# Optimization experiments

Hardware: AMD Instinct MI355X
Metric: run time of the kernel (lower is better)

## Reference

```python
import jax, jax.numpy as jnp
import numpy as np
from jax import lax

L, B, S, D, H = 2, 8, 2048, 1024, 1024
LOG_H0 = float(np.log(0.5))  # h0 = g(0) = 0.5


def _log_g(x):
    # log of g(x) = x + 0.5 if x >= 0 else sigmoid(x)
    return jnp.where(x >= 0, jnp.log(jnp.where(x >= 0, x + 0.5, 1.0)), -jax.nn.softplus(-x))


def _mingru_layer(x, Wz, bz, Wh, bh):
    # x: (B,S,D) -> (B,S,H) via log-space heinsen associative scan
    k = jnp.einsum('bsd,hd->bsh', x, Wz) + bz          # gate pre-activation
    log_z = -jax.nn.softplus(-k)                        # log sigmoid(k)
    log_coeffs = -jax.nn.softplus(k)                    # log (1 - sigmoid(k))
    pre_h = jnp.einsum('bsd,hd->bsh', x, Wh) + bh
    log_values = log_z + _log_g(pre_h)                  # log(z * h_tilde)
    Bq = x.shape[0]
    # prepend initial state: coeff 0 (log 1), value log(h0)
    log_coeffs = jnp.pad(log_coeffs, ((0, 0), (1, 0), (0, 0)))
    log_values = jnp.concatenate(
        [jnp.full((Bq, 1, log_values.shape[-1]), LOG_H0, dtype=log_values.dtype), log_values], axis=1)
    a_star = jnp.cumsum(log_coeffs, axis=1)
    log_h = a_star + lax.cumlogsumexp(log_values - a_star, axis=1)
    return jnp.exp(log_h)[:, 1:]


def setup_inputs() -> dict:
    key = jax.random.key(0)
    ks = jax.random.split(key, 5)
    stdv = 1.0 / np.sqrt(D)
    u = lambda k, shp: jax.random.uniform(k, shp, jnp.float32, -stdv, stdv)
    return {
        'x': jax.random.normal(ks[0], (B, S, D), jnp.float32),
        'Wz': u(ks[1], (L, H, D)),
        'bz': u(ks[2], (L, H)),
        'Wh': u(ks[3], (L, H, D)),
        'bh': u(ks[4], (L, H)),
    }


def reference(x, Wz, bz, Wh, bh):
    h = x
    for l in range(Wz.shape[0]):
        h = _mingru_layer(h, Wz[l], bz[l], Wh[l], bh[l])
    return h  # (B,S,H), last layer outputs
```

## Files before the change

kernel.cpp:

```cpp
#include <hip/hip_runtime.h>
#include <hip/hip_bf16.h>


#define L_ 2
#define B_ 8
#define S_ 2048
#define D_ 1024
#define H_ 1024
#define M_ (B_*S_)
#define NC 32
#define CL (S_/NC)

typedef __bf16    bf16x8 __attribute__((ext_vector_type(8)));
typedef float     f32x4  __attribute__((ext_vector_type(4)));
typedef _Float16  h2     __attribute__((ext_vector_type(2)));
typedef _Float16  h4     __attribute__((ext_vector_type(4)));

__device__ __forceinline__ ushort f2bf(float f) {
    union { __hip_bfloat16 h; ushort u; } c;
    c.h = __float2bfloat16(f);
    return c.u;
}

__device__ __forceinline__ void async16(const void* g, void* l) {
    __builtin_amdgcn_global_load_lds(
        (const __attribute__((address_space(1))) unsigned int*)g,
        (__attribute__((address_space(3))) unsigned int*)l, 16, 0, 0);
}

__global__ __launch_bounds__(256) void cast_f32_bf16(const float* __restrict__ in,
                                                     ushort* __restrict__ out, int n4) {
    int i = blockIdx.x * 256 + threadIdx.x;
    if (i >= n4) return;
    float4 v = ((const float4*)in)[i];
    ushort4 o;
    o.x = f2bf(v.x); o.y = f2bf(v.y); o.z = f2bf(v.z); o.w = f2bf(v.w);
    ((ushort4*)out)[i] = o;
}

#define SWZ(R, c) (((R) << 6) + ((((c) ^ ((R) & 7))) << 3))

__global__ __launch_bounds__(256) void gemm_fused(const ushort* __restrict__ A,
                                                  const ushort* __restrict__ Wz,
                                                  const ushort* __restrict__ Wh,
                                                  const float* __restrict__ bz,
                                                  const float* __restrict__ bh,
                                                  h2* __restrict__ cv,
                                                  float* __restrict__ Ac,
                                                  float* __restrict__ Bc)
{
    __shared__ __align__(16) ushort sm[16384];
    ushort* As = sm;
    ushort* Zs = sm + 8192;
    ushort* Hs = sm + 12288;

    const int t    = threadIdx.x;
    const int lane = t & 63;
    const int wave = t >> 6;
    const int xcd = (int)blockIdx.x & 7;
    const int k8  = (int)blockIdx.x >> 3;
    const int nblk = k8 & 15;
    const int mblk = ((k8 >> 4) << 3) + xcd;
    const int m0 = mblk * 128;
    const int n0 = nblk * 64;
    const int wm = (wave >> 1) * 64;
    const int wn = (wave & 1) * 32;

    const int srow   = lane >> 3;
    const int scol_g = (((lane & 7) ^ srow) << 3);

    f32x4 accz[4][2] = {};
    f32x4 acch[4][2] = {};
    const int lrow = lane & 15;
    const int lcq  = lane >> 4;

    for (int kb = 0; kb < D_; kb += 64) {
        __syncthreads();
        #pragma unroll
        for (int i = 0; i < 4; ++i) {
            int r = i*32 + wave*8;
            async16(&A[(size_t)(m0 + r + srow)*D_ + kb + scol_g], &As[r*64]);
        }
        #pragma unroll
        for (int i = 0; i < 2; ++i) {
            int r = i*32 + wave*8;
            async16(&Wz[(size_t)(n0 + r + srow)*D_ + kb + scol_g], &Zs[r*64]);
            async16(&Wh[(size_t)(n0 + r + srow)*D_ + kb + scol_g], &Hs[r*64]);
        }
        __syncthreads();
        #pragma unroll
        for (int kk = 0; kk < 64; kk += 32) {
            const int cq = (kk >> 3) + lcq;
            bf16x8 af[4];
            #pragma unroll
            for (int mt = 0; mt < 4; ++mt) {
                int R = wm + mt*16 + lrow;
                uint4 u = *(const uint4*)&As[SWZ(R, cq)];
                af[mt] = __builtin_bit_cast(bf16x8, u);
            }
            #pragma unroll
            for (int nt = 0; nt < 2; ++nt) {
                int R = wn + nt*16 + lrow;
                uint4 uz = *(const uint4*)&Zs[SWZ(R, cq)];
                uint4 uh = *(const uint4*)&Hs[SWZ(R, cq)];
                bf16x8 zb = __builtin_bit_cast(bf16x8, uz);
                bf16x8 hb = __builtin_bit_cast(bf16x8, uh);
                #pragma unroll
                for (int mt = 0; mt < 4; ++mt) {
                    accz[mt][nt] = __builtin_amdgcn_mfma_f32_16x16x32_bf16(af[mt], zb, accz[mt][nt], 0, 0, 0);
                    acch[mt][nt] = __builtin_amdgcn_mfma_f32_16x16x32_bf16(af[mt], hb, acch[mt][nt], 0, 0, 0);
                }
            }
        }
    }

    __syncthreads();
    float2* seg = (float2*)sm;

    const int colq = lane & 15;
    const int rowq = (lane >> 4) * 4;
    #pragma unroll
    for (int nt = 0; nt < 2; ++nt) {
        const int n = n0 + wn + nt*16 + colq;
        const float bzv = bz[n];
        const float bhv = bh[n];
        #pragma unroll
        for (int mt = 0; mt < 4; ++mt) {
            float a = 1.f, bb = 0.f;
            #pragma unroll
            for (int r = 0; r < 4; ++r) {
                const int m = m0 + wm + mt*16 + rowq + r;
                float k = accz[mt][nt][r] + bzv;
                float p = acch[mt][nt][r] + bhv;
                float e   = __expf(-fabsf(k));
                float inv = 1.0f / (1.0f + e);
                float z   = (k >= 0.f) ? inv     : e * inv;
                float c   = (k >= 0.f) ? e * inv : inv;
                float g;
                if (p >= 0.f) g = p + 0.5f;
                else { float eg = __expf(p); g = eg / (1.0f + eg); }
                float v = z * g;
                h2 hv; hv[0] = (_Float16)c; hv[1] = (_Float16)v;
                cv[(size_t)m * H_ + n] = hv;
                bb = fmaf(c, bb, v);
                a *= c;
            }
            const int sidx = (wm >> 2) + mt*4 + (rowq >> 2);
            seg[sidx*65 + wn + nt*16 + colq] = make_float2(a, bb);
        }
    }
    __syncthreads();
    if (t < 128) {
        const int col  = t & 63;
        const int half = t >> 6;
        float a = 1.f, bb = 0.f;
        #pragma unroll
        for (int s = 0; s < 16; ++s) {
            float2 e = seg[(half*16 + s)*65 + col];
            bb = fmaf(e.x, bb, e.y);
            a *= e.x;
        }
        const int b     = m0 >> 11;
        const int chunk = ((m0 >> 6) & (NC - 1)) + half;
        const int q = (b*NC + chunk)*H_ + n0 + col;
        Ac[q] = a; Bc[q] = bb;
    }
}

__global__ __launch_bounds__(256) void scan_chunk_combine(const float* __restrict__ Ac,
                                                          const float* __restrict__ Bc,
                                                          float* __restrict__ hin)
{
    int q = blockIdx.x * 256 + threadIdx.x;
    int h = q & (H_-1);
    int b = q >> 10;
    float hcur = 0.5f;
    #pragma unroll
    for (int c = 0; c < NC; ++c) {
        int idx = (b*NC + c)*H_ + h;
        hin[idx] = hcur;
        hcur = fmaf(Ac[idx], hcur, Bc[idx]);
    }
}

__global__ __launch_bounds__(256) void scan_emit(const h2* __restrict__ cv,
                                                 const float* __restrict__ hin,
                                                 float* __restrict__ outf,
                                                 ushort* __restrict__ outb,
                                                 const int write_bf16)
{
    int q = blockIdx.x * 256 + threadIdx.x;
    int hp = (q & 511) * 2;
    int c = (q >> 9) & (NC-1);
    int b = q >> 14;
    size_t base = (size_t)(b*S_ + c*CL) * H_ + hp;
    int qh = (b*NC + c)*H_ + hp;
    float h0 = hin[qh], h1 = hin[qh + 1];
    if (write_bf16) {
        #pragma unroll 4
        for (int tt = 0; tt < CL; ++tt) {
            h4 e = *(const h4*)&cv[base + (size_t)tt * H_];
            h0 = fmaf((float)e[0], h0, (float)e[1]);
            h1 = fmaf((float)e[2], h1, (float)e[3]);
            ushort2 o; o.x = f2bf(h0); o.y = f2bf(h1);
            *(ushort2*)&outb[base + (size_t)tt * H_] = o;
        }
    } else {
        #pragma unroll 4
        for (int tt = 0; tt < CL; ++tt) {
            h4 e = *(const h4*)&cv[base + (size_t)tt * H_];
            h0 = fmaf((float)e[0], h0, (float)e[1]);
            h1 = fmaf((float)e[2], h1, (float)e[3]);
            *(float2*)&outf[base + (size_t)tt * H_] = make_float2(h0, h1);
        }
    }
}

extern "C" void kernel_launch(void* const* d_in, const int* in_sizes, int n_in,
                              void* d_out, int out_size, void* d_ws, size_t ws_size,
                              hipStream_t stream)
{
    const float* x  = (const float*)d_in[0];
    const float* Wz = (const float*)d_in[1];
    const float* bz = (const float*)d_in[2];
    const float* Wh = (const float*)d_in[3];
    const float* bh = (const float*)d_in[4];
    float* out = (float*)d_out;

    ushort* xb  = (ushort*)d_ws;
    ushort* wzb = xb  + (size_t)M_*D_;
    ushort* whb = wzb + (size_t)L_*H_*D_;
    h2*     cv  = (h2*)(whb + (size_t)L_*H_*D_);
    float*  Ac  = (float*)(cv + (size_t)M_*H_);
    float*  Bc  = Ac + B_*NC*H_;
    float*  hin = Bc + B_*NC*H_;

    cast_f32_bf16<<<(M_*D_/4)/256, 256, 0, stream>>>(x, xb, M_*D_/4);
    cast_f32_bf16<<<(L_*H_*D_/4)/256, 256, 0, stream>>>(Wz, wzb, L_*H_*D_/4);
    cast_f32_bf16<<<(L_*H_*D_/4)/256, 256, 0, stream>>>(Wh, whb, L_*H_*D_/4);

    const int gemm_grid = (M_/128) * (H_/64);
    for (int l = 0; l < L_; ++l) {
        gemm_fused<<<gemm_grid, 256, 0, stream>>>(xb,
                                                  wzb + (size_t)l*H_*D_,
                                                  whb + (size_t)l*H_*D_,
                                                  bz + l*H_, bh + l*H_,
                                                  cv, Ac, Bc);
        scan_chunk_combine<<<(B_*H_)/256, 256, 0, stream>>>(Ac, Bc, hin);
        scan_emit<<<(B_*NC*H_/2)/256, 256, 0, stream>>>(cv, hin, out, xb, (l == 0) ? 1 : 0);
    }
}
```

Baseline: 340.8 us.

## Store gate coefficient/value pairs time-major per channel for vectorized writes and scan reads

The intermediate (coefficient, value) fp16 pairs move from a [b,t,h] layout to a [b,h,t] layout. The GEMM epilogue can then pack four consecutive timesteps into one 16-byte store instead of four scattered 4-byte stores. The scan kernel reads 16-byte runs along time for each channel. The catch is that adjacent threads in the scan now read addresses S apart, so each thread's loads are wide but not coalesced across the warp.

Measured after the change: 353.2 us. 3.7% more time.

```diff
diff --git a/kernel.cpp b/kernel.cpp
--- a/kernel.cpp
+++ b/kernel.cpp
@@ -14,7 +14,6 @@
 typedef __bf16    bf16x8 __attribute__((ext_vector_type(8)));
 typedef float     f32x4  __attribute__((ext_vector_type(4)));
 typedef _Float16  h2     __attribute__((ext_vector_type(2)));
-typedef _Float16  h4     __attribute__((ext_vector_type(4)));
 
 __device__ __forceinline__ ushort f2bf(float f) {
     union { __hip_bfloat16 h; ushort u; } c;
@@ -119,6 +118,8 @@
 
     const int colq = lane & 15;
     const int rowq = (lane >> 4) * 4;
+    const int bq   = m0 >> 11;
+    const int tb   = m0 & (S_-1);
     #pragma unroll
     for (int nt = 0; nt < 2; ++nt) {
         const int n = n0 + wn + nt*16 + colq;
@@ -127,9 +128,9 @@
         #pragma unroll
         for (int mt = 0; mt < 4; ++mt) {
             float a = 1.f, bb = 0.f;
+            union { h2 h[4]; uint4 u; } pk;
             #pragma unroll
             for (int r = 0; r < 4; ++r) {
-                const int m = m0 + wm + mt*16 + rowq + r;
                 float k = accz[mt][nt][r] + bzv;
                 float p = acch[mt][nt][r] + bhv;
                 float e   = __expf(-fabsf(k));
@@ -140,11 +141,12 @@
                 if (p >= 0.f) g = p + 0.5f;
                 else { float eg = __expf(p); g = eg / (1.0f + eg); }
                 float v = z * g;
-                h2 hv; hv[0] = (_Float16)c; hv[1] = (_Float16)v;
-                cv[(size_t)m * H_ + n] = hv;
+                pk.h[r][0] = (_Float16)c; pk.h[r][1] = (_Float16)v;
                 bb = fmaf(c, bb, v);
                 a *= c;
             }
+            const int tt = tb + wm + mt*16 + rowq;
+            *(uint4*)&cv[(size_t)(bq*H_ + n)*S_ + tt] = pk.u;
             const int sidx = (wm >> 2) + mt*4 + (rowq >> 2);
             seg[sidx*65 + wn + nt*16 + colq] = make_float2(a, bb);
         }
@@ -160,9 +162,8 @@
             bb = fmaf(e.x, bb, e.y);
             a *= e.x;
         }
-        const int b     = m0 >> 11;
         const int chunk = ((m0 >> 6) & (NC - 1)) + half;
-        const int q = (b*NC + chunk)*H_ + n0 + col;
+        const int q = (bq*NC + chunk)*H_ + n0 + col;
         Ac[q] = a; Bc[q] = bb;
     }
 }
@@ -191,27 +192,39 @@
 {
     int q = blockIdx.x * 256 + threadIdx.x;
     int hp = (q & 511) * 2;
-    int c = (q >> 9) & (NC-1);
-    int b = q >> 14;
-    size_t base = (size_t)(b*S_ + c*CL) * H_ + hp;
-    int qh = (b*NC + c)*H_ + hp;
-    float h0 = hin[qh], h1 = hin[qh + 1];
+    int c  = (q >> 9) & (NC-1);
+    int b  = q >> 14;
+    const h2* p0 = cv + (size_t)(b*H_ + hp    )*S_ + c*CL;
+    const h2* p1 = cv + (size_t)(b*H_ + hp + 1)*S_ + c*CL;
+    float2 hv = *(const float2*)&hin[(b*NC + c)*H_ + hp];
+    float h0 = hv.x, h1 = hv.y;
+    const size_t obase = (size_t)(b*S_ + c*CL)*H_ + hp;
     if (write_bf16) {
         #pragma unroll 4
-        for (int tt = 0; tt < CL; ++tt) {
-            h4 e = *(const h4*)&cv[base + (size_t)tt * H_];
-            h0 = fmaf((float)e[0], h0, (float)e[1]);
-            h1 = fmaf((float)e[2], h1, (float)e[3]);
-            ushort2 o; o.x = f2bf(h0); o.y = f2bf(h1);
-            *(ushort2*)&outb[base + (size_t)tt * H_] = o;
+        for (int i = 0; i < CL/4; ++i) {
+            union { uint4 u; h2 h[4]; } e0, e1;
+            e0.u = *(const uint4*)&p0[i*4];
+            e1.u = *(const uint4*)&p1[i*4];
+            #pragma unroll
+            for (int j = 0; j < 4; ++j) {
+                h0 = fmaf((float)e0.h[j][0], h0, (float)e0.h[j][1]);
+                h1 = fmaf((float)e1.h[j][0], h1, (float)e1.h[j][1]);
+                ushort2 o; o.x = f2bf(h0); o.y = f2bf(h1);
+                *(ushort2*)&outb[obase + (size_t)(i*4 + j)*H_] = o;
+            }
         }
     } else {
         #pragma unroll 4
-        for (int tt = 0; tt < CL; ++tt) {
-            h4 e = *(const h4*)&cv[base + (size_t)tt * H_];
-            h0 = fmaf((float)e[0], h0, (float)e[1]);
-            h1 = fmaf((float)e[2], h1, (float)e[3]);
-            *(float2*)&outf[base + (size_t)tt * H_] = make_float2(h0, h1);
+        for (int i = 0; i < CL/4; ++i) {
+            union { uint4 u; h2 h[4]; } e0, e1;
+            e0.u = *(const uint4*)&p0[i*4];
+            e1.u = *(const uint4*)&p1[i*4];
+            #pragma unroll
+            for (int j = 0; j < 4; ++j) {
+                h0 = fmaf((float)e0.h[j][0], h0, (float)e0.h[j][1]);
+                h1 = fmaf((float)e1.h[j][0], h1, (float)e1.h[j][1]);
+                *(float2*)&outf[obase + (size_t)(i*4 + j)*H_] = make_float2(h0, h1);
+            }
         }
     }
 }
```

## Stage GEMM epilogue cv through swizzled LDS for coalesced stores, double scan chunks

Applied to the files above, without the earlier changes.

The GEMM epilogue now writes the fp16 coefficient/value pairs into a swizzled LDS tile and then copies them out as 16-byte coalesced global stores, instead of scattered 4-byte stores. The chunk-summary partials are held in registers until LDS is free, and the scan chunk count doubles to 64, so all 256 threads reduce quarter-tiles and scan_emit gets more parallel chunks. The three cast kernels are merged into one launch. The costs are extra LDS passes and barriers in the epilogue, and a longer serial loop in the chunk-combine kernel.

Result: slower. 353.4 us (+3.7%).

```diff
diff --git a/kernel.cpp b/kernel.cpp
--- a/kernel.cpp
+++ b/kernel.cpp
@@ -8,13 +8,14 @@
 #define D_ 1024
 #define H_ 1024
 #define M_ (B_*S_)
-#define NC 32
+#define NC 64
 #define CL (S_/NC)
+#define XN4 (M_*D_/4)
+#define WN4 (L_*H_*D_/4)
 
 typedef __bf16    bf16x8 __attribute__((ext_vector_type(8)));
 typedef float     f32x4  __attribute__((ext_vector_type(4)));
 typedef _Float16  h2     __attribute__((ext_vector_type(2)));
-typedef _Float16  h4     __attribute__((ext_vector_type(4)));
 
 __device__ __forceinline__ ushort f2bf(float f) {
     union { __hip_bfloat16 h; ushort u; } c;
@@ -28,14 +29,21 @@
         (__attribute__((address_space(3))) unsigned int*)l, 16, 0, 0);
 }
 
-__global__ __launch_bounds__(256) void cast_f32_bf16(const float* __restrict__ in,
-                                                     ushort* __restrict__ out, int n4) {
+__global__ __launch_bounds__(256) void cast_all(const float* __restrict__ x,
+                                                const float* __restrict__ Wz,
+                                                const float* __restrict__ Wh,
+                                                ushort* __restrict__ xb,
+                                                ushort* __restrict__ wzb,
+                                                ushort* __restrict__ whb) {
     int i = blockIdx.x * 256 + threadIdx.x;
-    if (i >= n4) return;
-    float4 v = ((const float4*)in)[i];
+    const float* src; ushort* dst; int j;
+    if (i < XN4)            { src = x;  dst = xb;  j = i; }
+    else if (i < XN4 + WN4) { src = Wz; dst = wzb; j = i - XN4; }
+    else                    { src = Wh; dst = whb; j = i - XN4 - WN4; }
+    float4 v = ((const float4*)src)[j];
     ushort4 o;
     o.x = f2bf(v.x); o.y = f2bf(v.y); o.z = f2bf(v.z); o.w = f2bf(v.w);
-    ((ushort4*)out)[i] = o;
+    ((ushort4*)dst)[j] = o;
 }
 
 #define SWZ(R, c) (((R) << 6) + ((((c) ^ ((R) & 7))) << 3))
@@ -115,21 +123,27 @@
     }
 
     __syncthreads();
-    float2* seg = (float2*)sm;
+    h2* ldscv = (h2*)sm;
 
     const int colq = lane & 15;
     const int rowq = (lane >> 4) * 4;
+    const int bq   = m0 >> 11;
+    const int tb   = m0 & (S_-1);
+    float2 segreg[2][4];
     #pragma unroll
     for (int nt = 0; nt < 2; ++nt) {
-        const int n = n0 + wn + nt*16 + colq;
+        const int n_local = wn + nt*16 + colq;
+        const int n = n0 + n_local;
         const float bzv = bz[n];
         const float bhv = bh[n];
+        const int chunk4 = n_local >> 2;
+        const int within = n_local & 3;
         #pragma unroll
         for (int mt = 0; mt < 4; ++mt) {
             float a = 1.f, bb = 0.f;
             #pragma unroll
             for (int r = 0; r < 4; ++r) {
-                const int m = m0 + wm + mt*16 + rowq + r;
+                const int tl = wm + mt*16 + rowq + r;
                 float k = accz[mt][nt][r] + bzv;
                 float p = acch[mt][nt][r] + bhv;
                 float e   = __expf(-fabsf(k));
@@ -141,28 +155,47 @@
                 else { float eg = __expf(p); g = eg / (1.0f + eg); }
                 float v = z * g;
                 h2 hv; hv[0] = (_Float16)c; hv[1] = (_Float16)v;
-                cv[(size_t)m * H_ + n] = hv;
+                ldscv[tl*64 + ((chunk4 ^ (tl & 15)) << 2) + within] = hv;
                 bb = fmaf(c, bb, v);
                 a *= c;
             }
+            segreg[nt][mt] = make_float2(a, bb);
+        }
+    }
+    __syncthreads();
+    {
+        const uint4* l4 = (const uint4*)sm;
+        #pragma unroll
+        for (int i = 0; i < 8; ++i) {
+            int linear = i*256 + t;
+            int tl  = linear >> 4;
+            int c16 = linear & 15;
+            uint4 u = l4[tl*16 + (c16 ^ (tl & 15))];
+            *(uint4*)&cv[(size_t)(bq*S_ + tb + tl)*H_ + n0 + (c16 << 2)] = u;
+        }
+    }
+    __syncthreads();
+    float2* seg = (float2*)sm;
+    #pragma unroll
+    for (int nt = 0; nt < 2; ++nt)
+        #pragma unroll
+        for (int mt = 0; mt < 4; ++mt) {
             const int sidx = (wm >> 2) + mt*4 + (rowq >> 2);
-            seg[sidx*65 + wn + nt*16 + colq] = make_float2(a, bb);
-        }
-    }
-    __syncthreads();
-    if (t < 128) {
-        const int col  = t & 63;
-        const int half = t >> 6;
+            seg[sidx*65 + wn + nt*16 + colq] = segreg[nt][mt];
+        }
+    __syncthreads();
+    {
+        const int col     = t & 63;
+        const int quarter = t >> 6;
         float a = 1.f, bb = 0.f;
         #pragma unroll
-        for (int s = 0; s < 16; ++s) {
-            float2 e = seg[(half*16 + s)*65 + col];
+        for (int s = 0; s < 8; ++s) {
+            float2 e = seg[(quarter*8 + s)*65 + col];
             bb = fmaf(e.x, bb, e.y);
             a *= e.x;
         }
-        const int b     = m0 >> 11;
-        const int chunk = ((m0 >> 6) & (NC - 1)) + half;
-        const int q = (b*NC + chunk)*H_ + n0 + col;
+        const int chunk = (tb >> 5) + quarter;
+        const int q = (bq*NC + chunk)*H_ + n0 + col;
         Ac[q] = a; Bc[q] = bb;
     }
 }
@@ -191,26 +224,29 @@
 {
     int q = blockIdx.x * 256 + threadIdx.x;
     int hp = (q & 511) * 2;
-    int c = (q >> 9) & (NC-1);
-    int b = q >> 14;
+    int c  = (q >> 9) & (NC-1);
+    int b  = q >> 15;
     size_t base = (size_t)(b*S_ + c*CL) * H_ + hp;
-    int qh = (b*NC + c)*H_ + hp;
-    float h0 = hin[qh], h1 = hin[qh + 1];
+    float2 hv = *(const float2*)&hin[(b*NC + c)*H_ + hp];
+    float h0 = hv.x, h1 = hv.y;
+    const h2* p = cv + base;
     if (write_bf16) {
         #pragma unroll 4
         for (int tt = 0; tt < CL; ++tt) {
-            h4 e = *(const h4*)&cv[base + (size_t)tt * H_];
-            h0 = fmaf((float)e[0], h0, (float)e[1]);
-            h1 = fmaf((float)e[2], h1, (float)e[3]);
+            h2 e0 = p[(size_t)tt * H_];
+            h2 e1 = p[(size_t)tt * H_ + 1];
+            h0 = fmaf((float)e0[0], h0, (float)e0[1]);
+            h1 = fmaf((float)e1[0], h1, (float)e1[1]);
             ushort2 o; o.x = f2bf(h0); o.y = f2bf(h1);
             *(ushort2*)&outb[base + (size_t)tt * H_] = o;
         }
     } else {
         #pragma unroll 4
         for (int tt = 0; tt < CL; ++tt) {
-            h4 e = *(const h4*)&cv[base + (size_t)tt * H_];
-            h0 = fmaf((float)e[0], h0, (float)e[1]);
-            h1 = fmaf((float)e[2], h1, (float)e[3]);
+            h2 e0 = p[(size_t)tt * H_];
+            h2 e1 = p[(size_t)tt * H_ + 1];
+            h0 = fmaf((float)e0[0], h0, (float)e0[1]);
+            h1 = fmaf((float)e1[0], h1, (float)e1[1]);
             *(float2*)&outf[base + (size_t)tt * H_] = make_float2(h0, h1);
         }
     }
@@ -235,9 +271,7 @@
     float*  Bc  = Ac + B_*NC*H_;
     float*  hin = Bc + B_*NC*H_;
 
-    cast_f32_bf16<<<(M_*D_/4)/256, 256, 0, stream>>>(x, xb, M_*D_/4);
-    cast_f32_bf16<<<(L_*H_*D_/4)/256, 256, 0, stream>>>(Wz, wzb, L_*H_*D_/4);
-    cast_f32_bf16<<<(L_*H_*D_/4)/256, 256, 0, stream>>>(Wh, whb, L_*H_*D_/4);
+    cast_all<<<(XN4 + 2*WN4)/256, 256, 0, stream>>>(x, Wz, Wh, xb, wzb, whb);
 
     const int gemm_grid = (M_/128) * (H_/64);
     for (int l = 0; l < L_; ++l) {
```
